# Performance work log

Measured on AMD Instinct MI355X. Metric: run time of the kernel, lower is better.

## Reference

```python
import jax, jax.numpy as jnp
import numpy as np

C = 256
CQK = C // 8


def setup_inputs() -> dict:
    key = jax.random.key(0)
    ks = jax.random.split(key, 8)
    B, H, W = 4, 64, 64
    x = jax.random.normal(ks[0], (B, C, H, W), dtype=jnp.float32)
    # 1x1 conv weights are plain [out_c, in_c] matrices + bias
    sq = 1.0 / np.sqrt(C)
    Wq = jax.random.uniform(ks[1], (CQK, C), jnp.float32, -sq, sq)
    bq = jax.random.uniform(ks[2], (CQK,), jnp.float32, -sq, sq)
    Wk = jax.random.uniform(ks[3], (CQK, C), jnp.float32, -sq, sq)
    bk = jax.random.uniform(ks[4], (CQK,), jnp.float32, -sq, sq)
    Wv = jax.random.uniform(ks[5], (C, C), jnp.float32, -sq, sq)
    bv = jax.random.uniform(ks[6], (C,), jnp.float32, -sq, sq)
    gamma = jnp.zeros((1,), dtype=jnp.float32)
    return {"x": x, "Wq": Wq, "bq": bq, "Wk": Wk, "bk": bk, "Wv": Wv, "bv": bv, "gamma": gamma}


def reference(x, Wq, bq, Wk, bk, Wv, bv, gamma):
    B, Cc, H, W = x.shape
    N = H * W
    xf = x.reshape(B, Cc, N)  # [B, C, N]
    # 1x1 convs == channel GEMMs
    q = jnp.einsum('dc,bcn->bdn', Wq, xf) + bq[None, :, None]  # [B, C/8, N]
    k = jnp.einsum('dc,bcn->bdn', Wk, xf) + bk[None, :, None]  # [B, C/8, N]
    v = jnp.einsum('dc,bcn->bdn', Wv, xf) + bv[None, :, None]  # [B, C, N]
    # attention[b, i, j] = softmax_j( q_i . k_j )  (no scaling, as in source)
    attn = jax.nn.softmax(jnp.einsum('bdn,bdm->bnm', q, k), axis=-1)  # [B, N, N]
    # out = value @ attention  (note: NOT attention^T, faithful to source)
    out = jnp.einsum('bcn,bnm->bcm', v, attn)  # [B, C, N]
    out = out.reshape(B, Cc, H, W)
    return gamma[0] * out + x
```

## Files before the change

### kernel.cpp

```cpp
#include <hip/hip_runtime.h>
#include <hip/hip_bf16.h>


#define NB 4
#define CC 256
#define NN 4096
#define L2E 1.44269504088896340f

typedef short  short4v  __attribute__((ext_vector_type(4)));
typedef short  short8v  __attribute__((ext_vector_type(8)));
typedef __bf16 bf16x8   __attribute__((ext_vector_type(8)));
typedef float  f32x4    __attribute__((ext_vector_type(4)));
typedef float  f32x16   __attribute__((ext_vector_type(16)));
typedef unsigned long u64x2 __attribute__((ext_vector_type(2)));
typedef unsigned int u32;

#define AS1 __attribute__((address_space(1)))
#define AS3 __attribute__((address_space(3)))

static __device__ __forceinline__ void gload16(const void* g, void* l) {
  __builtin_amdgcn_global_load_lds((const AS1 u32*)g, (AS3 u32*)l, 16, 0, 0);
}

static __device__ __forceinline__ unsigned short f2bf(float f) {
  union { __bf16 h; unsigned short u; } v; v.h = (__bf16)f; return v.u;
}
static __device__ __forceinline__ float bf2f(unsigned short u) {
  union { unsigned u; float f; } v; v.u = (u32)u << 16; return v.f;
}

union FragU { short8v s; bf16x8 b; unsigned u[4]; };

static __device__ __forceinline__ bf16x8 ld_frag(const unsigned short* p) {
  FragU u; u.s = *(const short8v*)p; return u.b;
}

static __device__ __forceinline__ f32x16 zero16() {
  f32x16 v;
#pragma unroll
  for (int i = 0; i < 16; ++i) v[i] = 0.0f;
  return v;
}

static __device__ __forceinline__ f32x16 mfma32(bf16x8 a, bf16x8 b, f32x16 c) {
  return __builtin_amdgcn_mfma_f32_32x32x16_bf16(a, b, c, 0, 0, 0);
}

__global__ __launch_bounds__(256) void k_wcvt(
    const float* __restrict__ Wq, const float* __restrict__ Wk,
    const float* __restrict__ Wv, unsigned short* __restrict__ Wb)
{
  const int i4 = blockIdx.x * 256 + threadIdx.x;
  const int e = i4 * 4;
  const int row = e >> 8, c = e & 255;
  const float* src = (row < 32) ? (Wq + row * 256 + c)
                   : (row < 64) ? (Wk + (row - 32) * 256 + c)
                                : (Wv + (row - 64) * 256 + c);
  f32x4 v = *(const f32x4*)src;
  short4v s;
#pragma unroll
  for (int j = 0; j < 4; ++j) s[j] = (short)f2bf(v[j]);
  *(short4v*)(Wb + e) = s;
}

__global__ __launch_bounds__(256) void k_proj(
    const float* __restrict__ x, const unsigned short* __restrict__ Wb,
    const float* __restrict__ bq, const float* __restrict__ bk,
    const float* __restrict__ bv,
    unsigned short* __restrict__ Qt, unsigned short* __restrict__ Kt,
    unsigned char* __restrict__ V8)
{
  __shared__ unsigned short xs[32][268];
  const int t = threadIdx.x;
  const int b = blockIdx.y;
  const int n0 = blockIdx.x * 32;
  const int w = t >> 6, l = t & 63, h = l >> 5, col = l & 31;

  const float* xb = x + (size_t)b * CC * NN;
  {
    const int c_off = t >> 3, nl = 4 * (t & 7);
#pragma unroll
    for (int c0 = 0; c0 < CC; c0 += 32) {
      int c = c0 + c_off;
      f32x4 v4 = *(const f32x4*)(xb + (size_t)c * NN + n0 + nl);
#pragma unroll
      for (int j = 0; j < 4; ++j) xs[nl + j][c] = f2bf(v4[j]);
    }
  }
  __syncthreads();

  for (int f = w; f < 10; f += 4) {
    const float* bsrc; int rowbase; int mode; int wrow;
    if (f == 0)      { bsrc = bq; rowbase = 0;            mode = 0; wrow = 0; }
    else if (f == 1) { bsrc = bk; rowbase = 0;            mode = 1; wrow = 32; }
    else             { bsrc = bv; rowbase = (f - 2) * 32; mode = 2; wrow = 64 + rowbase; }

    f32x16 acc0 = zero16();
    const unsigned short* wr = Wb + (size_t)(wrow + col) * 256 + 8 * h;

#pragma unroll
    for (int k0 = 0; k0 < CC; k0 += 16) {
      FragU a;
      a.s = *(const short8v*)(wr + k0);
      const unsigned short* p0 = &xs[col][k0 + 8 * h];
      FragU b0;
      short4v t0a = *(const short4v*)p0, t0b = *(const short4v*)(p0 + 4);
#pragma unroll
      for (int j = 0; j < 4; ++j) { b0.s[j] = t0a[j]; b0.s[4 + j] = t0b[j]; }
      acc0 = mfma32(a.b, b0.b, acc0);
    }

    const int n = n0 + col;
#pragma unroll
    for (int q = 0; q < 4; ++q) {
      f32x4 bias4 = *(const f32x4*)(bsrc + rowbase + 8 * q + 4 * h);
      float vals[4];
#pragma unroll
      for (int i = 0; i < 4; ++i) vals[i] = acc0[4 * q + i] + bias4[i];
      if (mode == 2) {
        const size_t tb = (((size_t)b * (NN >> 4) + (n >> 4)) * 2 + ((n >> 3) & 1)) * CC * 8
                          + (n & 7);
        u32 w01 = __builtin_amdgcn_cvt_pk_fp8_f32(vals[0], vals[1], 0, false);
        u32 w23 = __builtin_amdgcn_cvt_pk_fp8_f32(vals[2], vals[3], 0, false);
        const int cb0 = rowbase + 8 * q + 4 * h;
        V8[tb + (size_t)(cb0 + 0) * 8] = (unsigned char)(w01 & 0xff);
        V8[tb + (size_t)(cb0 + 1) * 8] = (unsigned char)((w01 >> 8) & 0xff);
        V8[tb + (size_t)(cb0 + 2) * 8] = (unsigned char)(w23 & 0xff);
        V8[tb + (size_t)(cb0 + 3) * 8] = (unsigned char)((w23 >> 8) & 0xff);
      } else {
        unsigned short* dst = (mode == 0) ? Qt : Kt;
        const float scale = (mode == 0) ? L2E : 1.0f;
        short4v s4;
#pragma unroll
        for (int i = 0; i < 4; ++i) s4[i] = (short)f2bf(vals[i] * scale);
        *(short4v*)(dst + ((size_t)b * NN + n) * 32 + 8 * q + 4 * h) = s4;
      }
    }
  }
}

__global__ __launch_bounds__(256) void k_rowstats(
    const unsigned short* __restrict__ Qt, const unsigned short* __restrict__ Kt,
    float* __restrict__ cbias)
{
  __shared__ float ssum[4][32];
  const int t = threadIdx.x;
  const int w = t >> 6, l = t & 63, h = l >> 5, col = l & 31;
  const int b = blockIdx.y;
  const int n0 = blockIdx.x * 32;
  const unsigned short* Qb = Qt + (size_t)b * NN * 32;
  const unsigned short* Kb = Kt + (size_t)b * NN * 32;

  bf16x8 bq0 = ld_frag(Qb + (size_t)(n0 + col) * 32 + 8 * h);
  bf16x8 bq1 = ld_frag(Qb + (size_t)(n0 + col) * 32 + 16 + 8 * h);

  float acc = 0.0f;
  const int mbase = w * (NN / 4);
#pragma unroll 2
  for (int mt = 0; mt < 32; ++mt) {
    const int m0 = mbase + mt * 32;
    bf16x8 ak0 = ld_frag(Kb + (size_t)(m0 + col) * 32 + 8 * h);
    bf16x8 ak1 = ld_frag(Kb + (size_t)(m0 + col) * 32 + 16 + 8 * h);
    f32x16 S = zero16();
    S = mfma32(ak0, bq0, S);
    S = mfma32(ak1, bq1, S);
    float p0 = 0.0f, p1 = 0.0f, p2 = 0.0f, p3 = 0.0f;
#pragma unroll
    for (int r = 0; r < 4; ++r) {
      p0 += __builtin_amdgcn_exp2f(S[r]);
      p1 += __builtin_amdgcn_exp2f(S[4 + r]);
      p2 += __builtin_amdgcn_exp2f(S[8 + r]);
      p3 += __builtin_amdgcn_exp2f(S[12 + r]);
    }
    acc += (p0 + p1) + (p2 + p3);
  }
  acc += __shfl_xor(acc, 32);

  if (l < 32) ssum[w][l] = acc;
  __syncthreads();

  if (t < 32) {
    float s = (ssum[0][t] + ssum[1][t]) + (ssum[2][t] + ssum[3][t]);
    cbias[(size_t)b * NN + n0 + t] = -__builtin_amdgcn_logf(s);
  }
}

__global__ __launch_bounds__(512) void k_attn_out(
    const unsigned short* __restrict__ Qt, const unsigned short* __restrict__ Kt,
    const unsigned char* __restrict__ V8,
    const float* __restrict__ cbias,
    unsigned short* __restrict__ pout,
    int nsplit, int nlen)
{
  __shared__ __align__(16) char qbuf[2][4][2048];
  __shared__ __align__(16) char vbuf[3][4][8192];
  __shared__ __align__(16) char ebuf[2][4][4096];

  const int wg = (int)blockIdx.x;
  const int chunk = (int)gridDim.x >> 3;
  const int id2 = (wg & 7) * chunk + (wg >> 3);
  const int per_b = 32 * nsplit;
  const int b = id2 / per_b;
  const int rem = id2 - b * per_b;
  const int ns = rem >> 5;
  const int m0 = (rem & 31) * 128;
  const int nbeg = ns * nlen;

  const int t = threadIdx.x;
  const int w = t >> 6, l = t & 63, h = l >> 5, col = l & 31;
  const int mfp = w & 3;
  const int ccons = (w & 3) * 64;

  const unsigned short* Kb = Kt + (size_t)b * NN * 32;
  const float* cb = cbias + (size_t)b * NN + nbeg;

  bf16x8 bk0 = ld_frag(Kb + (size_t)(m0 + 32 * mfp + col) * 32 + 8 * h);
  bf16x8 bk1 = ld_frag(Kb + (size_t)(m0 + 32 * mfp + col) * 32 + 16 + 8 * h);

  const int ll = l & 15;
  const size_t gqoff = (size_t)(((w & 1) * 16 + ll) * 64 + ((w >> 1) & 1) * 16
                                + (w >> 2) * 32);
  const char* qsrc = (const char*)Qt + ((size_t)b * NN + nbeg) * 64 + gqoff;
  const char* vsrc = (const char*)V8 + ((size_t)b * (NN >> 4) + (nbeg >> 4)) * 4096
                     + (size_t)t * 16;

  f32x16 acc[4][2];
#pragma unroll
  for (int mf = 0; mf < 4; ++mf)
#pragma unroll
    for (int cf = 0; cf < 2; ++cf) acc[mf][cf] = zero16();

  const int J = nlen >> 7;

#pragma unroll
  for (int u = 0; u < 4; ++u) {
    if (ll == l) gload16(qsrc + (size_t)u * 2048, &qbuf[0][u][w * 256]);
    gload16(vsrc + (size_t)u * 8192, &vbuf[0][u][w * 1024]);
  }
  __syncthreads();

  for (int j = 0; j <= J; ++j) {
    if (j + 1 < J) {
      const size_t qoff = (size_t)(4 * j + 4) * 2048;
      const size_t voff = (size_t)(4 * j + 4) * 8192;
      const int qs = (j + 1) & 1, vs = (j + 1) % 3;
#pragma unroll
      for (int u = 0; u < 4; ++u) {
        if (ll == l) gload16(qsrc + qoff + (size_t)u * 2048, &qbuf[qs][u][w * 256]);
        gload16(vsrc + voff + (size_t)u * 8192, &vbuf[vs][u][w * 1024]);
      }
    }

    if (w < 4) {
      if (j < J) {
#pragma unroll
        for (int u = 0; u < 4; ++u) {
          const char* qb = &qbuf[j & 1][u][0];
          FragU fq0, fq1;
          fq0.s = *(const short8v*)(qb + l * 16);
          fq1.s = *(const short8v*)(qb + 1024 + l * 16);
          f32x16 S = zero16();
          S = mfma32(fq0.b, bk0, S);
          S = mfma32(fq1.b, bk1, S);

          float e[16];
          const float* cbi = cb + (4 * j + u) * 32;
#pragma unroll
          for (int q = 0; q < 4; ++q) {
            f32x4 cb4 = *(const f32x4*)(cbi + 8 * q + 4 * h);
#pragma unroll
            for (int i = 0; i < 4; ++i)
              e[4 * q + i] = __builtin_amdgcn_exp2f(S[4 * q + i] + cb4[i]);
          }
          u32 wA = __builtin_amdgcn_cvt_pk_fp8_f32(e[0], e[1], 0, false);
          wA = __builtin_amdgcn_cvt_pk_fp8_f32(e[2], e[3], wA, true);
          u32 wB = __builtin_amdgcn_cvt_pk_fp8_f32(e[4], e[5], 0, false);
          wB = __builtin_amdgcn_cvt_pk_fp8_f32(e[6], e[7], wB, true);
          u32 wC = __builtin_amdgcn_cvt_pk_fp8_f32(e[8], e[9], 0, false);
          wC = __builtin_amdgcn_cvt_pk_fp8_f32(e[10], e[11], wC, true);
          u32 wD = __builtin_amdgcn_cvt_pk_fp8_f32(e[12], e[13], 0, false);
          wD = __builtin_amdgcn_cvt_pk_fp8_f32(e[14], e[15], wD, true);
          asm("v_permlane32_swap_b32 %0, %1" : "+v"(wA), "+v"(wB));
          asm("v_permlane32_swap_b32 %0, %1" : "+v"(wC), "+v"(wD));
          u64x2 ev;
          ev[0] = ((unsigned long)wB << 32) | wA;
          ev[1] = ((unsigned long)wD << 32) | wC;
          *(u64x2*)(&ebuf[j & 1][u][mfp * 1024 + l * 16]) = ev;
        }
      }
    } else {
      if (j > 0) {
        const int pv = (j + 2) % 3;
        __builtin_amdgcn_s_setprio(1);
#pragma unroll
        for (int u = 0; u < 4; ++u) {
          const char* vb = &vbuf[pv][u][h * 2048 + (ccons + col) * 8];
          long v00 = *(const long*)(vb);
          long v01 = *(const long*)(vb + 256);
          long v10 = *(const long*)(vb + 4096);
          long v11 = *(const long*)(vb + 4096 + 256);
          const char* eb = &ebuf[(j - 1) & 1][u][l * 16];
          u64x2 ev0 = *(const u64x2*)(eb);
          u64x2 ev1 = *(const u64x2*)(eb + 1024);
          u64x2 ev2 = *(const u64x2*)(eb + 2048);
          u64x2 ev3 = *(const u64x2*)(eb + 3072);
          acc[0][0] = __builtin_amdgcn_mfma_f32_32x32x16_fp8_fp8((long)ev0[0], v00, acc[0][0], 0, 0, 0);
          acc[1][0] = __builtin_amdgcn_mfma_f32_32x32x16_fp8_fp8((long)ev1[0], v00, acc[1][0], 0, 0, 0);
          acc[2][0] = __builtin_amdgcn_mfma_f32_32x32x16_fp8_fp8((long)ev2[0], v00, acc[2][0], 0, 0, 0);
          acc[3][0] = __builtin_amdgcn_mfma_f32_32x32x16_fp8_fp8((long)ev3[0], v00, acc[3][0], 0, 0, 0);
          acc[0][1] = __builtin_amdgcn_mfma_f32_32x32x16_fp8_fp8((long)ev0[0], v01, acc[0][1], 0, 0, 0);
          acc[1][1] = __builtin_amdgcn_mfma_f32_32x32x16_fp8_fp8((long)ev1[0], v01, acc[1][1], 0, 0, 0);
          acc[2][1] = __builtin_amdgcn_mfma_f32_32x32x16_fp8_fp8((long)ev2[0], v01, acc[2][1], 0, 0, 0);
          acc[3][1] = __builtin_amdgcn_mfma_f32_32x32x16_fp8_fp8((long)ev3[0], v01, acc[3][1], 0, 0, 0);
          acc[0][0] = __builtin_amdgcn_mfma_f32_32x32x16_fp8_fp8((long)ev0[1], v10, acc[0][0], 0, 0, 0);
          acc[1][0] = __builtin_amdgcn_mfma_f32_32x32x16_fp8_fp8((long)ev1[1], v10, acc[1][0], 0, 0, 0);
          acc[2][0] = __builtin_amdgcn_mfma_f32_32x32x16_fp8_fp8((long)ev2[1], v10, acc[2][0], 0, 0, 0);
          acc[3][0] = __builtin_amdgcn_mfma_f32_32x32x16_fp8_fp8((long)ev3[1], v10, acc[3][0], 0, 0, 0);
          acc[0][1] = __builtin_amdgcn_mfma_f32_32x32x16_fp8_fp8((long)ev0[1], v11, acc[0][1], 0, 0, 0);
          acc[1][1] = __builtin_amdgcn_mfma_f32_32x32x16_fp8_fp8((long)ev1[1], v11, acc[1][1], 0, 0, 0);
          acc[2][1] = __builtin_amdgcn_mfma_f32_32x32x16_fp8_fp8((long)ev2[1], v11, acc[2][1], 0, 0, 0);
          acc[3][1] = __builtin_amdgcn_mfma_f32_32x32x16_fp8_fp8((long)ev3[1], v11, acc[3][1], 0, 0, 0);
        }
        __builtin_amdgcn_s_setprio(0);
      }
    }

    if (j < J) __syncthreads();
  }

  if (w >= 4) {
    unsigned short* pb = pout + (((size_t)ns * NB + b) * NN + m0) * CC + ccons;
#pragma unroll
    for (int mf = 0; mf < 4; ++mf)
#pragma unroll
      for (int cf = 0; cf < 2; ++cf)
#pragma unroll
        for (int r = 0; r < 16; ++r) {
          int mloc = 32 * mf + (r & 3) + 8 * (r >> 2) + 4 * h;
          pb[(size_t)mloc * CC + 32 * cf + col] = f2bf(acc[mf][cf][r]);
        }
  }
}

__global__ __launch_bounds__(256) void k_comb(
    const unsigned short* __restrict__ pout, const float* __restrict__ x,
    const float* __restrict__ gamma, float* __restrict__ out, int nsplit)
{
  __shared__ float ld[64][65];
  const size_t STRIDE = (size_t)NB * CC * NN;
  const int t = threadIdx.x;
  const int m0 = blockIdx.x * 64, c0 = blockIdx.y * 64, b = blockIdx.z;
  const int ci = t & 63, mo = t >> 6;

  const unsigned short* pb = pout + ((size_t)b * NN + m0) * CC + c0;
#pragma unroll
  for (int rep = 0; rep < 16; ++rep) {
    const int mi = 4 * rep + mo;
    float s = bf2f(pb[(size_t)mi * CC + ci]);
    for (int ns = 1; ns < nsplit; ++ns)
      s += bf2f(pb[ns * STRIDE + (size_t)mi * CC + ci]);
    ld[mi][ci] = s;
  }
  __syncthreads();

  const float g = gamma[0];
  const int mi2 = t & 63;
#pragma unroll
  for (int rep = 0; rep < 16; ++rep) {
    const int cj = 4 * rep + mo;
    const size_t idx = ((size_t)b * CC + c0 + cj) * NN + m0 + mi2;
    out[idx] = g * ld[mi2][cj] + x[idx];
  }
}

extern "C" void kernel_launch(void* const* d_in, const int* in_sizes, int n_in,
                              void* d_out, int out_size, void* d_ws, size_t ws_size,
                              hipStream_t stream) {
  const float* x     = (const float*)d_in[0];
  const float* Wq    = (const float*)d_in[1];
  const float* bq    = (const float*)d_in[2];
  const float* Wk    = (const float*)d_in[3];
  const float* bk    = (const float*)d_in[4];
  const float* Wv    = (const float*)d_in[5];
  const float* bv    = (const float*)d_in[6];
  const float* gamma = (const float*)d_in[7];
  float* out = (float*)d_out;

  char* ws = (char*)d_ws;
  unsigned short* Qt = (unsigned short*)(ws);
  unsigned short* Kt = (unsigned short*)(ws + (1u << 20));
  unsigned char*  V8 = (unsigned char*)(ws + (2u << 20));
  unsigned short* Wb = (unsigned short*)(ws + (6u << 20));
  float* cbias = (float*)(ws + (10u << 20) + (2u << 18));
  const size_t POUT_OFF = (11u << 20);
  unsigned short* pout = (unsigned short*)(ws + POUT_OFF);
  const size_t PART_BYTES = (size_t)NB * CC * NN * 2;

  int nsplit = (ws_size >= POUT_OFF + 2 * PART_BYTES) ? 2 : 1;

  k_wcvt<<<dim3(80), 256, 0, stream>>>(Wq, Wk, Wv, Wb);
  k_proj<<<dim3(NN / 32, NB), 256, 0, stream>>>(x, Wb, bq, bk, bv, Qt, Kt, V8);
  k_rowstats<<<dim3(NN / 32, NB), 256, 0, stream>>>(Qt, Kt, cbias);
  k_attn_out<<<dim3(128 * nsplit), 512, 0, stream>>>(
      Qt, Kt, V8, cbias, pout, nsplit, NN / nsplit);
  k_comb<<<dim3(NN / 64, CC / 64, NB), 256, 0, stream>>>(pout, x, gamma, out, nsplit);
}
```

Before: 98.16 us.

## Widen attention block to 12 waves and software-pipeline QK MFMA ahead of exp

Raises the k_attn_out block from 8 to 12 waves so that 8 consumer waves each own 32 output channels instead of 64, halving accumulator registers per wave. The n-step shrinks from 128 to 64 rows and the Q buffer becomes triple-buffered. Producer waves now compute the next step's QK scores before the current step's exp/fp8 conversion, so MFMA latency overlaps with the transcendental work. Each wave also issues its own loads (Q only from producers, V only from consumers). In exchange there are twice as many barriers per row of work, and more threads per block may lower occupancy or register headroom.

Result: slower. 127.9 us (+30.2%).

```diff
diff --git a/kernel.cpp b/kernel.cpp
--- a/kernel.cpp
+++ b/kernel.cpp
@@ -185,16 +185,16 @@
   }
 }
 
-__global__ __launch_bounds__(512) void k_attn_out(
+__global__ __launch_bounds__(768) void k_attn_out(
     const unsigned short* __restrict__ Qt, const unsigned short* __restrict__ Kt,
     const unsigned char* __restrict__ V8,
     const float* __restrict__ cbias,
     unsigned short* __restrict__ pout,
     int nsplit, int nlen)
 {
-  __shared__ __align__(16) char qbuf[2][4][2048];
-  __shared__ __align__(16) char vbuf[3][4][8192];
-  __shared__ __align__(16) char ebuf[2][4][4096];
+  __shared__ __align__(16) char qbuf[3][2][2048];
+  __shared__ __align__(16) char vbuf[3][2][8192];
+  __shared__ __align__(16) char ebuf[2][2][4096];
 
   const int wg = (int)blockIdx.x;
   const int chunk = (int)gridDim.x >> 3;
@@ -208,8 +208,9 @@
 
   const int t = threadIdx.x;
   const int w = t >> 6, l = t & 63, h = l >> 5, col = l & 31;
+  const bool isP = (w < 4);
   const int mfp = w & 3;
-  const int ccons = (w & 3) * 64;
+  const int ccons = (w - 4) * 32;
 
   const unsigned short* Kb = Kt + (size_t)b * NN * 32;
   const float* cb = cbias + (size_t)b * NN + nbeg;
@@ -217,60 +218,77 @@
   bf16x8 bk0 = ld_frag(Kb + (size_t)(m0 + 32 * mfp + col) * 32 + 8 * h);
   bf16x8 bk1 = ld_frag(Kb + (size_t)(m0 + 32 * mfp + col) * 32 + 16 + 8 * h);
 
-  const int ll = l & 15;
-  const size_t gqoff = (size_t)(((w & 1) * 16 + ll) * 64 + ((w >> 1) & 1) * 16
-                                + (w >> 2) * 32);
+  const size_t gqoff = (size_t)((l & 31) * 64 + (w & 1) * 16 + (w >> 1) * 32);
   const char* qsrc = (const char*)Qt + ((size_t)b * NN + nbeg) * 64 + gqoff;
   const char* vsrc = (const char*)V8 + ((size_t)b * (NN >> 4) + (nbeg >> 4)) * 4096
-                     + (size_t)t * 16;
-
-  f32x16 acc[4][2];
-#pragma unroll
-  for (int mf = 0; mf < 4; ++mf)
-#pragma unroll
-    for (int cf = 0; cf < 2; ++cf) acc[mf][cf] = zero16();
-
-  const int J = nlen >> 7;
-
-#pragma unroll
-  for (int u = 0; u < 4; ++u) {
-    if (ll == l) gload16(qsrc + (size_t)u * 2048, &qbuf[0][u][w * 256]);
-    gload16(vsrc + (size_t)u * 8192, &vbuf[0][u][w * 1024]);
+                     + (size_t)(w - 4) * 1024 + (size_t)l * 16;
+
+  f32x16 acc[4];
+#pragma unroll
+  for (int mf = 0; mf < 4; ++mf) acc[mf] = zero16();
+
+  f32x16 Ssave[2], Snew[2];
+
+  const int J = nlen >> 6;
+
+  if (isP) {
+    if (l < 32) {
+      gload16(qsrc, &qbuf[0][0][w * 512]);
+      gload16(qsrc + 2048, &qbuf[0][1][w * 512]);
+      gload16(qsrc + 2 * 2048, &qbuf[1][0][w * 512]);
+      gload16(qsrc + 3 * 2048, &qbuf[1][1][w * 512]);
+    }
+  } else {
+    gload16(vsrc, &vbuf[0][0][(w - 4) * 1024]);
+    gload16(vsrc + 8192, &vbuf[0][1][(w - 4) * 1024]);
   }
   __syncthreads();
 
+  if (isP) {
+#pragma unroll
+    for (int u = 0; u < 2; ++u) {
+      const char* qb = &qbuf[0][u][0];
+      FragU fq0, fq1;
+      fq0.s = *(const short8v*)(qb + l * 16);
+      fq1.s = *(const short8v*)(qb + 1024 + l * 16);
+      f32x16 S = zero16();
+      S = mfma32(fq0.b, bk0, S);
+      Ssave[u] = mfma32(fq1.b, bk1, S);
+    }
+  }
+
   for (int j = 0; j <= J; ++j) {
-    if (j + 1 < J) {
-      const size_t qoff = (size_t)(4 * j + 4) * 2048;
-      const size_t voff = (size_t)(4 * j + 4) * 8192;
-      const int qs = (j + 1) & 1, vs = (j + 1) % 3;
-#pragma unroll
-      for (int u = 0; u < 4; ++u) {
-        if (ll == l) gload16(qsrc + qoff + (size_t)u * 2048, &qbuf[qs][u][w * 256]);
-        gload16(vsrc + voff + (size_t)u * 8192, &vbuf[vs][u][w * 1024]);
-      }
-    }
-
-    if (w < 4) {
+    if (isP) {
+      if (j + 2 < J && l < 32) {
+        const size_t qoff = (size_t)(2 * (j + 2)) * 2048;
+        const int qs = (j + 2) % 3;
+        gload16(qsrc + qoff, &qbuf[qs][0][w * 512]);
+        gload16(qsrc + qoff + 2048, &qbuf[qs][1][w * 512]);
+      }
       if (j < J) {
-#pragma unroll
-        for (int u = 0; u < 4; ++u) {
-          const char* qb = &qbuf[j & 1][u][0];
-          FragU fq0, fq1;
-          fq0.s = *(const short8v*)(qb + l * 16);
-          fq1.s = *(const short8v*)(qb + 1024 + l * 16);
-          f32x16 S = zero16();
-          S = mfma32(fq0.b, bk0, S);
-          S = mfma32(fq1.b, bk1, S);
-
+        if (j + 1 < J) {
+          const int qs = (j + 1) % 3;
+#pragma unroll
+          for (int u = 0; u < 2; ++u) {
+            const char* qb = &qbuf[qs][u][0];
+            FragU fq0, fq1;
+            fq0.s = *(const short8v*)(qb + l * 16);
+            fq1.s = *(const short8v*)(qb + 1024 + l * 16);
+            f32x16 S = zero16();
+            S = mfma32(fq0.b, bk0, S);
+            Snew[u] = mfma32(fq1.b, bk1, S);
+          }
+        }
+#pragma unroll
+        for (int u = 0; u < 2; ++u) {
           float e[16];
-          const float* cbi = cb + (4 * j + u) * 32;
+          const float* cbi = cb + (2 * j + u) * 32;
 #pragma unroll
           for (int q = 0; q < 4; ++q) {
             f32x4 cb4 = *(const f32x4*)(cbi + 8 * q + 4 * h);
 #pragma unroll
             for (int i = 0; i < 4; ++i)
-              e[4 * q + i] = __builtin_amdgcn_exp2f(S[4 * q + i] + cb4[i]);
+              e[4 * q + i] = __builtin_amdgcn_exp2f(Ssave[u][4 * q + i] + cb4[i]);
           }
           u32 wA = __builtin_amdgcn_cvt_pk_fp8_f32(e[0], e[1], 0, false);
           wA = __builtin_amdgcn_cvt_pk_fp8_f32(e[2], e[3], wA, true);
@@ -287,39 +305,36 @@
           ev[1] = ((unsigned long)wD << 32) | wC;
           *(u64x2*)(&ebuf[j & 1][u][mfp * 1024 + l * 16]) = ev;
         }
+        if (j + 1 < J) { Ssave[0] = Snew[0]; Ssave[1] = Snew[1]; }
       }
     } else {
+      if (j + 1 < J) {
+        const size_t voff = (size_t)(2 * (j + 1)) * 8192;
+        const int vs = (j + 1) % 3;
+        gload16(vsrc + voff, &vbuf[vs][0][(w - 4) * 1024]);
+        gload16(vsrc + voff + 8192, &vbuf[vs][1][(w - 4) * 1024]);
+      }
       if (j > 0) {
         const int pv = (j + 2) % 3;
         __builtin_amdgcn_s_setprio(1);
 #pragma unroll
-        for (int u = 0; u < 4; ++u) {
+        for (int u = 0; u < 2; ++u) {
           const char* vb = &vbuf[pv][u][h * 2048 + (ccons + col) * 8];
-          long v00 = *(const long*)(vb);
-          long v01 = *(const long*)(vb + 256);
-          long v10 = *(const long*)(vb + 4096);
-          long v11 = *(const long*)(vb + 4096 + 256);
+          long v0 = *(const long*)(vb);
+          long v1 = *(const long*)(vb + 4096);
           const char* eb = &ebuf[(j - 1) & 1][u][l * 16];
           u64x2 ev0 = *(const u64x2*)(eb);
           u64x2 ev1 = *(const u64x2*)(eb + 1024);
           u64x2 ev2 = *(const u64x2*)(eb + 2048);
           u64x2 ev3 = *(const u64x2*)(eb + 3072);
-          acc[0][0] = __builtin_amdgcn_mfma_f32_32x32x16_fp8_fp8((long)ev0[0], v00, acc[0][0], 0, 0, 0);
-          acc[1][0] = __builtin_amdgcn_mfma_f32_32x32x16_fp8_fp8((long)ev1[0], v00, acc[1][0], 0, 0, 0);
-          acc[2][0] = __builtin_amdgcn_mfma_f32_32x32x16_fp8_fp8((long)ev2[0], v00, acc[2][0], 0, 0, 0);
-          acc[3][0] = __builtin_amdgcn_mfma_f32_32x32x16_fp8_fp8((long)ev3[0], v00, acc[3][0], 0, 0, 0);
-          acc[0][1] = __builtin_amdgcn_mfma_f32_32x32x16_fp8_fp8((long)ev0[0], v01, acc[0][1], 0, 0, 0);
-          acc[1][1] = __builtin_amdgcn_mfma_f32_32x32x16_fp8_fp8((long)ev1[0], v01, acc[1][1], 0, 0, 0);
-          acc[2][1] = __builtin_amdgcn_mfma_f32_32x32x16_fp8_fp8((long)ev2[0], v01, acc[2][1], 0, 0, 0);
-          acc[3][1] = __builtin_amdgcn_mfma_f32_32x32x16_fp8_fp8((long)ev3[0], v01, acc[3][1], 0, 0, 0);
-          acc[0][0] = __builtin_amdgcn_mfma_f32_32x32x16_fp8_fp8((long)ev0[1], v10, acc[0][0], 0, 0, 0);
-          acc[1][0] = __builtin_amdgcn_mfma_f32_32x32x16_fp8_fp8((long)ev1[1], v10, acc[1][0], 0, 0, 0);
-          acc[2][0] = __builtin_amdgcn_mfma_f32_32x32x16_fp8_fp8((long)ev2[1], v10, acc[2][0], 0, 0, 0);
-          acc[3][0] = __builtin_amdgcn_mfma_f32_32x32x16_fp8_fp8((long)ev3[1], v10, acc[3][0], 0, 0, 0);
-          acc[0][1] = __builtin_amdgcn_mfma_f32_32x32x16_fp8_fp8((long)ev0[1], v11, acc[0][1], 0, 0, 0);
-          acc[1][1] = __builtin_amdgcn_mfma_f32_32x32x16_fp8_fp8((long)ev1[1], v11, acc[1][1], 0, 0, 0);
-          acc[2][1] = __builtin_amdgcn_mfma_f32_32x32x16_fp8_fp8((long)ev2[1], v11, acc[2][1], 0, 0, 0);
-          acc[3][1] = __builtin_amdgcn_mfma_f32_32x32x16_fp8_fp8((long)ev3[1], v11, acc[3][1], 0, 0, 0);
+          acc[0] = __builtin_amdgcn_mfma_f32_32x32x16_fp8_fp8((long)ev0[0], v0, acc[0], 0, 0, 0);
+          acc[1] = __builtin_amdgcn_mfma_f32_32x32x16_fp8_fp8((long)ev1[0], v0, acc[1], 0, 0, 0);
+          acc[2] = __builtin_amdgcn_mfma_f32_32x32x16_fp8_fp8((long)ev2[0], v0, acc[2], 0, 0, 0);
+          acc[3] = __builtin_amdgcn_mfma_f32_32x32x16_fp8_fp8((long)ev3[0], v0, acc[3], 0, 0, 0);
+          acc[0] = __builtin_amdgcn_mfma_f32_32x32x16_fp8_fp8((long)ev0[1], v1, acc[0], 0, 0, 0);
+          acc[1] = __builtin_amdgcn_mfma_f32_32x32x16_fp8_fp8((long)ev1[1], v1, acc[1], 0, 0, 0);
+          acc[2] = __builtin_amdgcn_mfma_f32_32x32x16_fp8_fp8((long)ev2[1], v1, acc[2], 0, 0, 0);
+          acc[3] = __builtin_amdgcn_mfma_f32_32x32x16_fp8_fp8((long)ev3[1], v1, acc[3], 0, 0, 0);
         }
         __builtin_amdgcn_s_setprio(0);
       }
@@ -328,17 +343,15 @@
     if (j < J) __syncthreads();
   }
 
-  if (w >= 4) {
+  if (!isP) {
     unsigned short* pb = pout + (((size_t)ns * NB + b) * NN + m0) * CC + ccons;
 #pragma unroll
     for (int mf = 0; mf < 4; ++mf)
 #pragma unroll
-      for (int cf = 0; cf < 2; ++cf)
-#pragma unroll
-        for (int r = 0; r < 16; ++r) {
-          int mloc = 32 * mf + (r & 3) + 8 * (r >> 2) + 4 * h;
-          pb[(size_t)mloc * CC + 32 * cf + col] = f2bf(acc[mf][cf][r]);
-        }
+      for (int r = 0; r < 16; ++r) {
+        int mloc = 32 * mf + (r & 3) + 8 * (r >> 2) + 4 * h;
+        pb[(size_t)mloc * CC + col] = f2bf(acc[mf][r]);
+      }
   }
 }
 
@@ -401,7 +414,7 @@
   k_wcvt<<<dim3(80), 256, 0, stream>>>(Wq, Wk, Wv, Wb);
   k_proj<<<dim3(NN / 32, NB), 256, 0, stream>>>(x, Wb, bq, bk, bv, Qt, Kt, V8);
   k_rowstats<<<dim3(NN / 32, NB), 256, 0, stream>>>(Qt, Kt, cbias);
-  k_attn_out<<<dim3(128 * nsplit), 512, 0, stream>>>(
+  k_attn_out<<<dim3(128 * nsplit), 768, 0, stream>>>(
       Qt, Kt, V8, cbias, pout, nsplit, NN / nsplit);
   k_comb<<<dim3(NN / 64, CC / 64, NB), 256, 0, stream>>>(pout, x, gamma, out, nsplit);
 }
```

## Halve attention output tile to 64 rows with 2 producer and 4 consumer waves

Applied to the files above, without the earlier changes.

Reworks k_attn_out to cover 64 output positions per workgroup instead of 128, using 2 producer waves that compute exp scores and 4 consumer waves that run the fp8 MFMA accumulation, for 384 threads per block. The grid doubles (to 512 blocks when nsplit is 2) and LDS per block shrinks, aiming for more blocks in flight and better occupancy across CUs. In exchange, each block reuses its V tile over fewer output rows, so V traffic from L2 doubles, the producer-to-consumer wave ratio changes, and accumulator registers per consumer wave are halved.

New measurement: 114.4 us. 1.16x slower.

```diff
diff --git a/kernel.cpp b/kernel.cpp
--- a/kernel.cpp
+++ b/kernel.cpp
@@ -185,31 +185,32 @@
   }
 }
 
-__global__ __launch_bounds__(512) void k_attn_out(
+__global__ __launch_bounds__(384) void k_attn_out(
     const unsigned short* __restrict__ Qt, const unsigned short* __restrict__ Kt,
     const unsigned char* __restrict__ V8,
     const float* __restrict__ cbias,
     unsigned short* __restrict__ pout,
     int nsplit, int nlen)
 {
-  __shared__ __align__(16) char qbuf[2][4][2048];
-  __shared__ __align__(16) char vbuf[3][4][8192];
-  __shared__ __align__(16) char ebuf[2][4][4096];
+  __shared__ __align__(16) char qbuf[2][2][2048];
+  __shared__ __align__(16) char vbuf[3][2][8192];
+  __shared__ __align__(16) char ebuf[2][2][2048];
 
   const int wg = (int)blockIdx.x;
   const int chunk = (int)gridDim.x >> 3;
   const int id2 = (wg & 7) * chunk + (wg >> 3);
-  const int per_b = 32 * nsplit;
+  const int per_b = 64 * nsplit;
   const int b = id2 / per_b;
   const int rem = id2 - b * per_b;
-  const int ns = rem >> 5;
-  const int m0 = (rem & 31) * 128;
+  const int ns = rem >> 6;
+  const int m0 = (rem & 63) * 64;
   const int nbeg = ns * nlen;
 
   const int t = threadIdx.x;
   const int w = t >> 6, l = t & 63, h = l >> 5, col = l & 31;
-  const int mfp = w & 3;
-  const int ccons = (w & 3) * 64;
+  const bool isP = (w < 2);
+  const int mfp = w & 1;
+  const int ccons = (w - 2) * 64;
 
   const unsigned short* Kb = Kt + (size_t)b * NN * 32;
   const float* cb = cbias + (size_t)b * NN + nbeg;
@@ -217,44 +218,51 @@
   bf16x8 bk0 = ld_frag(Kb + (size_t)(m0 + 32 * mfp + col) * 32 + 8 * h);
   bf16x8 bk1 = ld_frag(Kb + (size_t)(m0 + 32 * mfp + col) * 32 + 16 + 8 * h);
 
-  const int ll = l & 15;
-  const size_t gqoff = (size_t)(((w & 1) * 16 + ll) * 64 + ((w >> 1) & 1) * 16
-                                + (w >> 2) * 32);
+  const size_t gqoff = (size_t)((l & 31) * 64 + (l >> 5) * 16 + w * 32);
   const char* qsrc = (const char*)Qt + ((size_t)b * NN + nbeg) * 64 + gqoff;
+  const int cw = w - 2;
   const char* vsrc = (const char*)V8 + ((size_t)b * (NN >> 4) + (nbeg >> 4)) * 4096
-                     + (size_t)t * 16;
-
-  f32x16 acc[4][2];
-#pragma unroll
-  for (int mf = 0; mf < 4; ++mf)
+                     + (size_t)(cw * 64 + l) * 16;
+
+  f32x16 acc[2][2];
+#pragma unroll
+  for (int mf = 0; mf < 2; ++mf)
 #pragma unroll
     for (int cf = 0; cf < 2; ++cf) acc[mf][cf] = zero16();
 
-  const int J = nlen >> 7;
-
-#pragma unroll
-  for (int u = 0; u < 4; ++u) {
-    if (ll == l) gload16(qsrc + (size_t)u * 2048, &qbuf[0][u][w * 256]);
-    gload16(vsrc + (size_t)u * 8192, &vbuf[0][u][w * 1024]);
+  const int J = nlen >> 6;
+
+  if (isP) {
+    gload16(qsrc, &qbuf[0][0][(w * 64 + l) * 16]);
+    gload16(qsrc + 2048, &qbuf[0][1][(w * 64 + l) * 16]);
+  } else {
+    gload16(vsrc, &vbuf[0][0][(size_t)(cw * 64 + l) * 16]);
+    gload16(vsrc + 4096, &vbuf[0][0][(size_t)(cw * 64 + l) * 16 + 4096]);
+    gload16(vsrc + 8192, &vbuf[0][1][(size_t)(cw * 64 + l) * 16]);
+    gload16(vsrc + 8192 + 4096, &vbuf[0][1][(size_t)(cw * 64 + l) * 16 + 4096]);
   }
   __syncthreads();
 
   for (int j = 0; j <= J; ++j) {
     if (j + 1 < J) {
-      const size_t qoff = (size_t)(4 * j + 4) * 2048;
-      const size_t voff = (size_t)(4 * j + 4) * 8192;
       const int qs = (j + 1) & 1, vs = (j + 1) % 3;
-#pragma unroll
-      for (int u = 0; u < 4; ++u) {
-        if (ll == l) gload16(qsrc + qoff + (size_t)u * 2048, &qbuf[qs][u][w * 256]);
-        gload16(vsrc + voff + (size_t)u * 8192, &vbuf[vs][u][w * 1024]);
+      if (isP) {
+        const size_t qoff = (size_t)(2 * j + 2) * 2048;
+        gload16(qsrc + qoff, &qbuf[qs][0][(w * 64 + l) * 16]);
+        gload16(qsrc + qoff + 2048, &qbuf[qs][1][(w * 64 + l) * 16]);
+      } else {
+        const size_t voff = (size_t)(2 * j + 2) * 8192;
+        gload16(vsrc + voff, &vbuf[vs][0][(size_t)(cw * 64 + l) * 16]);
+        gload16(vsrc + voff + 4096, &vbuf[vs][0][(size_t)(cw * 64 + l) * 16 + 4096]);
+        gload16(vsrc + voff + 8192, &vbuf[vs][1][(size_t)(cw * 64 + l) * 16]);
+        gload16(vsrc + voff + 8192 + 4096, &vbuf[vs][1][(size_t)(cw * 64 + l) * 16 + 4096]);
       }
     }
 
-    if (w < 4) {
+    if (isP) {
       if (j < J) {
 #pragma unroll
-        for (int u = 0; u < 4; ++u) {
+        for (int u = 0; u < 2; ++u) {
           const char* qb = &qbuf[j & 1][u][0];
           FragU fq0, fq1;
           fq0.s = *(const short8v*)(qb + l * 16);
@@ -264,7 +272,7 @@
           S = mfma32(fq1.b, bk1, S);
 
           float e[16];
-          const float* cbi = cb + (4 * j + u) * 32;
+          const float* cbi = cb + (2 * j + u) * 32;
 #pragma unroll
           for (int q = 0; q < 4; ++q) {
             f32x4 cb4 = *(const f32x4*)(cbi + 8 * q + 4 * h);
@@ -293,7 +301,7 @@
         const int pv = (j + 2) % 3;
         __builtin_amdgcn_s_setprio(1);
 #pragma unroll
-        for (int u = 0; u < 4; ++u) {
+        for (int u = 0; u < 2; ++u) {
           const char* vb = &vbuf[pv][u][h * 2048 + (ccons + col) * 8];
           long v00 = *(const long*)(vb);
           long v01 = *(const long*)(vb + 256);
@@ -302,24 +310,14 @@
           const char* eb = &ebuf[(j - 1) & 1][u][l * 16];
           u64x2 ev0 = *(const u64x2*)(eb);
           u64x2 ev1 = *(const u64x2*)(eb + 1024);
-          u64x2 ev2 = *(const u64x2*)(eb + 2048);
-          u64x2 ev3 = *(const u64x2*)(eb + 3072);
           acc[0][0] = __builtin_amdgcn_mfma_f32_32x32x16_fp8_fp8((long)ev0[0], v00, acc[0][0], 0, 0, 0);
           acc[1][0] = __builtin_amdgcn_mfma_f32_32x32x16_fp8_fp8((long)ev1[0], v00, acc[1][0], 0, 0, 0);
-          acc[2][0] = __builtin_amdgcn_mfma_f32_32x32x16_fp8_fp8((long)ev2[0], v00, acc[2][0], 0, 0, 0);
-          acc[3][0] = __builtin_amdgcn_mfma_f32_32x32x16_fp8_fp8((long)ev3[0], v00, acc[3][0], 0, 0, 0);
           acc[0][1] = __builtin_amdgcn_mfma_f32_32x32x16_fp8_fp8((long)ev0[0], v01, acc[0][1], 0, 0, 0);
           acc[1][1] = __builtin_amdgcn_mfma_f32_32x32x16_fp8_fp8((long)ev1[0], v01, acc[1][1], 0, 0, 0);
-          acc[2][1] = __builtin_amdgcn_mfma_f32_32x32x16_fp8_fp8((long)ev2[0], v01, acc[2][1], 0, 0, 0);
-          acc[3][1] = __builtin_amdgcn_mfma_f32_32x32x16_fp8_fp8((long)ev3[0], v01, acc[3][1], 0, 0, 0);
           acc[0][0] = __builtin_amdgcn_mfma_f32_32x32x16_fp8_fp8((long)ev0[1], v10, acc[0][0], 0, 0, 0);
           acc[1][0] = __builtin_amdgcn_mfma_f32_32x32x16_fp8_fp8((long)ev1[1], v10, acc[1][0], 0, 0, 0);
-          acc[2][0] = __builtin_amdgcn_mfma_f32_32x32x16_fp8_fp8((long)ev2[1], v10, acc[2][0], 0, 0, 0);
-          acc[3][0] = __builtin_amdgcn_mfma_f32_32x32x16_fp8_fp8((long)ev3[1], v10, acc[3][0], 0, 0, 0);
           acc[0][1] = __builtin_amdgcn_mfma_f32_32x32x16_fp8_fp8((long)ev0[1], v11, acc[0][1], 0, 0, 0);
           acc[1][1] = __builtin_amdgcn_mfma_f32_32x32x16_fp8_fp8((long)ev1[1], v11, acc[1][1], 0, 0, 0);
-          acc[2][1] = __builtin_amdgcn_mfma_f32_32x32x16_fp8_fp8((long)ev2[1], v11, acc[2][1], 0, 0, 0);
-          acc[3][1] = __builtin_amdgcn_mfma_f32_32x32x16_fp8_fp8((long)ev3[1], v11, acc[3][1], 0, 0, 0);
         }
         __builtin_amdgcn_s_setprio(0);
       }
@@ -328,10 +326,10 @@
     if (j < J) __syncthreads();
   }
 
-  if (w >= 4) {
+  if (!isP) {
     unsigned short* pb = pout + (((size_t)ns * NB + b) * NN + m0) * CC + ccons;
 #pragma unroll
-    for (int mf = 0; mf < 4; ++mf)
+    for (int mf = 0; mf < 2; ++mf)
 #pragma unroll
       for (int cf = 0; cf < 2; ++cf)
 #pragma unroll
@@ -401,7 +399,7 @@
   k_wcvt<<<dim3(80), 256, 0, stream>>>(Wq, Wk, Wv, Wb);
   k_proj<<<dim3(NN / 32, NB), 256, 0, stream>>>(x, Wb, bq, bk, bv, Qt, Kt, V8);
   k_rowstats<<<dim3(NN / 32, NB), 256, 0, stream>>>(Qt, Kt, cbias);
-  k_attn_out<<<dim3(128 * nsplit), 512, 0, stream>>>(
+  k_attn_out<<<dim3(NB * 64 * nsplit), 384, 0, stream>>>(
       Qt, Kt, V8, cbias, pout, nsplit, NN / nsplit);
   k_comb<<<dim3(NN / 64, CC / 64, NB), 256, 0, stream>>>(pout, x, gamma, out, nsplit);
 }
```
